# Kernel tuning notes

Hardware: AMD Instinct MI355X
Metric: run time of the kernel (lower is better)

## Reference

```python
import jax, jax.numpy as jnp
import numpy as np
from jax import lax

B, N, T, H, E, D, K = 2, 1024, 4096, 256, 2, 2, 9


def angle2vector(a):
    return jnp.stack([jnp.sin(a), jnp.cos(a)], axis=-1)


def setup_inputs() -> dict:
    key = jax.random.key(0)
    ks = jax.random.split(key, 16)
    s = jnp.float32(0.05)
    return {
        "x": jax.random.normal(ks[0], (B, N, T), jnp.float32),
        "z": jax.random.uniform(ks[1], (B, T, E, D), jnp.float32, 0.0, 2.0 * np.pi),
        # encoder: depthwise conv (groups=N) then two 1x1 convs
        "dw_w": jax.random.normal(ks[2], (N, 1, K), jnp.float32) * s,
        "dw_b": jax.random.normal(ks[3], (N,), jnp.float32) * s,
        "w1": jax.random.normal(ks[4], (H, N), jnp.float32) * s,
        "b1": jax.random.normal(ks[5], (H,), jnp.float32) * s,
        "w2": jax.random.normal(ks[6], (H, H), jnp.float32) * s,
        "b2": jax.random.normal(ks[7], (H,), jnp.float32) * s,
        # heads (1x1 convs)
        "wm": jax.random.normal(ks[8], (E * D * 2, H), jnp.float32) * s,
        "bm": jax.random.normal(ks[9], (E * D * 2,), jnp.float32) * s,
        "wv": jax.random.normal(ks[10], (E * D, H), jnp.float32) * s,
        "bv": jax.random.normal(ks[11], (E * D,), jnp.float32) * s,
        # feature basis / readout params
        "receptive_fields": jax.random.uniform(ks[12], (N, E, D), jnp.float32, 0.0, 2.0 * np.pi),
        "ensemble_weights": jax.random.normal(ks[13], (N, E), jnp.float32),
        "final_scale": jax.random.normal(ks[14], (N,), jnp.float32) * s,
        "log_tuning_width": jnp.full((1,), np.log(2.0), jnp.float32),
    }


def reference(x, z, dw_w, dw_b, w1, b1, w2, b2, wm, bm, wv, bv,
              receptive_fields, ensemble_weights, final_scale, log_tuning_width):
    # ---- encoder ----
    # depthwise conv1d, kernel_size=K, padding='same', groups=N
    h = lax.conv_general_dilated(
        x, dw_w, window_strides=(1,), padding="SAME",
        feature_group_count=N, dimension_numbers=("NCH", "OIH", "NCH"))
    h = h + dw_b[None, :, None]
    h = jax.nn.relu(jnp.einsum("hn,bnt->bht", w1, h) + b1[None, :, None])
    h = jax.nn.relu(jnp.einsum("gh,bht->bgt", w2, h) + b2[None, :, None])

    # ---- heads ----
    mu = jnp.einsum("oh,bht->bot", wm, h) + bm[None, :, None]  # [B, E*D*2, T]
    mu = mu.transpose(0, 2, 1).reshape(B, T, E, D, 2)
    logvar = jnp.einsum("oh,bht->bot", wv, h) + bv[None, :, None]  # [B, E*D, T]
    logvar = logvar.transpose(0, 2, 1).reshape(B, T, E, D)
    # normalize encodings onto unit circle
    mu = mu / jnp.sqrt(jnp.sum(mu ** 2, axis=-1, keepdims=True))

    # ---- feature basis ('bump') ----
    zv = angle2vector(z)                     # [B, T, E, D, 2]
    rfv = angle2vector(receptive_fields)     # [N, E, D, 2]
    diff = zv[:, :, None] - rfv[None, None]  # [B, T, N, E, D, 2]
    dist = jnp.sum(diff ** 2, axis=(4, 5))   # [B, T, N, E]
    response = jnp.exp(-dist / jnp.exp(log_tuning_width))  # nonlinearity='exp'

    # ---- ensemble-weighted readout ----
    ew = jax.nn.softmax(ensemble_weights, axis=1)  # [N, E]
    responses = jnp.einsum("btne,ne->btn", response, ew)
    responses = responses * jnp.exp(final_scale)[None, None]
    responses = responses.transpose(0, 2, 1)  # [B, N, T]
    return responses, z, mu, logvar
```

## Files before the change

kernel.cpp:

```cpp
#include <hip/hip_runtime.h>
#include <hip/hip_bf16.h>

#define B_ 2
#define N_ 1024
#define T_ 4096
#define H_ 256
#define ROWS_ 8192

typedef float f32x4 __attribute__((ext_vector_type(4)));
typedef __bf16 bf16x8 __attribute__((ext_vector_type(8)));

__device__ __forceinline__ void gl16(const void* g, void* l) {
  __builtin_amdgcn_global_load_lds(
      (const __attribute__((address_space(1))) void*)g,
      (__attribute__((address_space(3))) void*)l, 16, 0, 0);
}

__global__ __launch_bounds__(256) void cvt_split(
    const float* __restrict__ w1, const float* __restrict__ w2,
    __bf16* __restrict__ w1h, __bf16* __restrict__ w1l,
    __bf16* __restrict__ w2h, __bf16* __restrict__ w2l) {
  int i = blockIdx.x * 256 + threadIdx.x;
  if (i < 262144) {
    float v = w1[i];
    __bf16 h = (__bf16)v;
    w1h[i] = h;
    w1l[i] = (__bf16)(v - (float)h);
  } else {
    int j = i - 262144;
    float v = w2[j];
    __bf16 h = (__bf16)v;
    w2h[j] = h;
    w2l[j] = (__bf16)(v - (float)h);
  }
}

__global__ __launch_bounds__(256) void dwconv_t(
    const float* __restrict__ x, const float* __restrict__ w,
    const float* __restrict__ bias, __bf16* __restrict__ h0h,
    __bf16* __restrict__ h0l) {
  __shared__ float xs[64][76];
  const int tid = threadIdx.x;
  const int t0 = blockIdx.x * 64;
  const int n0 = blockIdx.y * 64;
  const int b = blockIdx.z;
  for (int i = tid; i < 64 * 72; i += 256) {
    int rr = i / 72, cc = i % 72;
    int tt = t0 - 4 + cc;
    xs[rr][cc] = (tt >= 0 && tt < T_) ? x[((size_t)(b * N_ + n0 + rr)) * T_ + tt] : 0.f;
  }
  const int nl = tid & 63;
  const int tg = tid >> 6;
  float wr[9];
  #pragma unroll
  for (int k = 0; k < 9; ++k) wr[k] = w[(n0 + nl) * 9 + k];
  const float bb = bias[n0 + nl];
  __syncthreads();
  float win[24];
  #pragma unroll
  for (int c = 0; c < 6; ++c)
    *(f32x4*)&win[c * 4] = *(const f32x4*)&xs[nl][tg * 16 + c * 4];
  const size_t obase = ((size_t)b * T_ + t0 + tg * 16) * N_ + n0 + nl;
  #pragma unroll
  for (int j = 0; j < 16; ++j) {
    float acc = bb;
    #pragma unroll
    for (int k = 0; k < 9; ++k) acc = fmaf(win[j + k], wr[k], acc);
    __bf16 h = (__bf16)acc;
    h0h[obase + (size_t)j * N_] = h;
    h0l[obase + (size_t)j * N_] = (__bf16)(acc - (float)h);
  }
}

__global__ __launch_bounds__(512) void encoder_fused(
    const __bf16* __restrict__ Ah, const __bf16* __restrict__ Al,
    const __bf16* __restrict__ W1h, const __bf16* __restrict__ W1l,
    const float* __restrict__ b1,
    const __bf16* __restrict__ W2h, const __bf16* __restrict__ W2l,
    const float* __restrict__ b2,
    const float* __restrict__ wm, const float* __restrict__ bm,
    const float* __restrict__ wv, const float* __restrict__ bv,
    float* __restrict__ out_mu, float* __restrict__ out_lv) {
  __shared__ __attribute__((aligned(16))) char smem[126976];
  char* const ASB = smem;
  char* const WSB = smem + 8192;
  char* const H1B = smem + 73728;
  float* const WMV = (float*)(smem + 106496);
  float* const H2S = (float*)(smem + 8192);

  const int tid = threadIdx.x;
  const int row0 = blockIdx.x * 32;
  const int lane = tid & 63;
  const int wid = tid >> 6;
  const int wt = (wid >> 2) * 16;
  const int wg = (wid & 3) * 64;
  const int lr = lane & 15;
  const int ls = lane >> 4;

  if (tid < 256) {
    #pragma unroll
    for (int i = 0; i < 8; ++i) WMV[tid * 20 + i] = wm[i * 256 + tid];
    #pragma unroll
    for (int i = 0; i < 4; ++i) WMV[tid * 20 + 8 + i] = wv[i * 256 + tid];
  }

  float b1g[4], b2g[4];
  #pragma unroll
  for (int ni = 0; ni < 4; ++ni) {
    b1g[ni] = b1[wg + ni * 16 + lr];
    b2g[ni] = b2[wg + ni * 16 + lr];
  }

  const int a_pl = tid >> 7;
  const int a_idx = tid & 127;
  const int a_r = a_idx >> 2;
  const int a_c = (a_idx & 3) ^ ((a_r >> 1) & 3);
  const __bf16* a_src = (a_pl ? Al : Ah) + (size_t)(row0 + a_r) * 1024 + a_c * 8;
  char* const a_dst = ASB + a_pl * 2048 + a_idx * 16;

  auto STAGE_A = [&](int buf, int kt) {
    if (tid < 256) gl16(a_src + kt * 32, a_dst + buf * 4096);
  };
  auto STAGE_W = [&](int buf, int k0, const __bf16* Wh, const __bf16* Wl, int K) {
    #pragma unroll
    for (int j = 0; j < 4; ++j) {
      const int s = tid + j * 512;
      const int pl = s >> 10;
      const int idx = s & 1023;
      const int g = idx >> 2;
      const int c = (idx & 3) ^ ((g >> 1) & 3);
      gl16((pl ? Wl : Wh) + (size_t)g * K + k0 + c * 8, WSB + buf * 32768 + s * 16);
    }
  };
  auto FR_A = [&](int cur, int pl, int r) {
    return *(const bf16x8*)(ASB + cur * 4096 + pl * 2048 + r * 64 +
                            (ls ^ ((r >> 1) & 3)) * 16);
  };
  auto FR_W = [&](int cur, int pl, int g) {
    return *(const bf16x8*)(WSB + cur * 32768 + pl * 16384 + g * 64 +
                            (ls ^ ((g >> 1) & 3)) * 16);
  };

  f32x4 acc[4];
  #pragma unroll
  for (int i = 0; i < 4; ++i) acc[i] = (f32x4)0.f;

  STAGE_A(0, 0);
  STAGE_W(0, 0, W1h, W1l, 1024);
  __syncthreads();
  for (int kt = 0; kt < 32; ++kt) {
    const int cur = kt & 1;
    if (kt + 1 < 32) {
      STAGE_A(cur ^ 1, kt + 1);
      STAGE_W(cur ^ 1, (kt + 1) * 32, W1h, W1l, 1024);
    }
    bf16x8 ah = FR_A(cur, 0, wt + lr);
    bf16x8 al = FR_A(cur, 1, wt + lr);
    #pragma unroll
    for (int ni = 0; ni < 4; ++ni) {
      bf16x8 wh = FR_W(cur, 0, wg + ni * 16 + lr);
      bf16x8 wl = FR_W(cur, 1, wg + ni * 16 + lr);
      acc[ni] = __builtin_amdgcn_mfma_f32_16x16x32_bf16(ah, wh, acc[ni], 0, 0, 0);
      acc[ni] = __builtin_amdgcn_mfma_f32_16x16x32_bf16(ah, wl, acc[ni], 0, 0, 0);
      acc[ni] = __builtin_amdgcn_mfma_f32_16x16x32_bf16(al, wh, acc[ni], 0, 0, 0);
    }
    __syncthreads();
  }

  #pragma unroll
  for (int ni = 0; ni < 4; ++ni) {
    const int g = wg + ni * 16 + lr;
    const int c = g >> 3;
    #pragma unroll
    for (int reg = 0; reg < 4; ++reg) {
      const int t = wt + ls * 4 + reg;
      float v = fmaxf(acc[ni][reg] + b1g[ni], 0.f);
      __bf16 h = (__bf16)v;
      const int off = t * 512 + ((c ^ (t & 7)) * 16) + (g & 7) * 2;
      *(__bf16*)(H1B + off) = h;
      *(__bf16*)(H1B + 16384 + off) = (__bf16)(v - (float)h);
    }
    acc[ni] = (f32x4)0.f;
  }
  STAGE_W(0, 0, W2h, W2l, 256);
  __syncthreads();

  for (int kt = 0; kt < 8; ++kt) {
    const int cur = kt & 1;
    if (kt + 1 < 8) STAGE_W(cur ^ 1, (kt + 1) * 32, W2h, W2l, 256);
    const int t = wt + lr;
    const int ca = ((kt * 4 + ls) ^ (t & 7)) * 16;
    bf16x8 ah = *(const bf16x8*)(H1B + t * 512 + ca);
    bf16x8 al = *(const bf16x8*)(H1B + 16384 + t * 512 + ca);
    #pragma unroll
    for (int ni = 0; ni < 4; ++ni) {
      bf16x8 wh = FR_W(cur, 0, wg + ni * 16 + lr);
      bf16x8 wl = FR_W(cur, 1, wg + ni * 16 + lr);
      acc[ni] = __builtin_amdgcn_mfma_f32_16x16x32_bf16(ah, wh, acc[ni], 0, 0, 0);
      acc[ni] = __builtin_amdgcn_mfma_f32_16x16x32_bf16(ah, wl, acc[ni], 0, 0, 0);
      acc[ni] = __builtin_amdgcn_mfma_f32_16x16x32_bf16(al, wh, acc[ni], 0, 0, 0);
    }
    __syncthreads();
  }

  #pragma unroll
  for (int ni = 0; ni < 4; ++ni) {
    const int g = wg + ni * 16 + lr;
    #pragma unroll
    for (int reg = 0; reg < 4; ++reg) {
      const int t = wt + ls * 4 + reg;
      H2S[t * 264 + g] = fmaxf(acc[ni][reg] + b2g[ni], 0.f);
    }
  }
  __syncthreads();

  const int ht = tid >> 4;
  const int sub = tid & 15;
  float s[12];
  #pragma unroll
  for (int o = 0; o < 12; ++o) s[o] = 0.f;
  #pragma unroll
  for (int j = 0; j < 16; ++j) {
    const int k = sub + j * 16;
    const float hv = H2S[ht * 264 + k];
    const float* wp = &WMV[k * 20];
    #pragma unroll
    for (int o = 0; o < 12; ++o) s[o] = fmaf(wp[o], hv, s[o]);
  }
  #pragma unroll
  for (int o = 0; o < 12; ++o) {
    s[o] += __shfl_xor(s[o], 1);
    s[o] += __shfl_xor(s[o], 2);
    s[o] += __shfl_xor(s[o], 4);
    s[o] += __shfl_xor(s[o], 8);
  }
  const size_t row = row0 + ht;
  if (sub == 0) {
    float mm[8];
    #pragma unroll
    for (int ed = 0; ed < 4; ++ed) {
      float m0 = s[ed * 2] + bm[ed * 2];
      float m1 = s[ed * 2 + 1] + bm[ed * 2 + 1];
      float inv = 1.f / sqrtf(m0 * m0 + m1 * m1);
      mm[ed * 2] = m0 * inv;
      mm[ed * 2 + 1] = m1 * inv;
    }
    *(float4*)&out_mu[row * 8] = make_float4(mm[0], mm[1], mm[2], mm[3]);
    *(float4*)&out_mu[row * 8 + 4] = make_float4(mm[4], mm[5], mm[6], mm[7]);
  } else if (sub == 1) {
    *(float4*)&out_lv[row * 4] =
        make_float4(s[8] + bv[0], s[9] + bv[1], s[10] + bv[2], s[11] + bv[3]);
  }
}

__global__ __launch_bounds__(256) void resp_kernel(
    const float* __restrict__ z, const float* __restrict__ rf,
    const float* __restrict__ ew, const float* __restrict__ fs,
    const float* __restrict__ ltw, float* __restrict__ out,
    float* __restrict__ out_z) {
  __shared__ float s_sin[32][4], s_cos[32][4], s_w[32][2];
  const int tid = threadIdx.x;
  const int tc = blockIdx.x;
  const int nc = blockIdx.y;
  const int b = blockIdx.z;
  if (tid < 128) {
    int nl = tid >> 2, ed = tid & 3;
    float a = rf[(nc * 32 + nl) * 4 + ed];
    s_sin[nl][ed] = sinf(a);
    s_cos[nl][ed] = cosf(a);
  }
  if (tid < 32) {
    int n = nc * 32 + tid;
    float e0 = ew[n * 2], e1 = ew[n * 2 + 1];
    float m = fmaxf(e0, e1);
    float x0 = expf(e0 - m), x1 = expf(e1 - m);
    float sc = expf(fs[n]) / (x0 + x1);
    s_w[tid][0] = x0 * sc;
    s_w[tid][1] = x1 * sc;
  }
  __syncthreads();
  const int t = tc * 1024 + (tid >> 6) * 256 + (tid & 63) * 4;
  const float inv_tw = expf(-ltw[0]);
  float sz[16], cz[16];
  #pragma unroll
  for (int j = 0; j < 4; ++j) {
    float4 zv = *(const float4*)&z[((size_t)b * T_ + t + j) * 4];
    if (nc == 0) *(float4*)&out_z[((size_t)b * T_ + t + j) * 4] = zv;
    sz[j * 4 + 0] = sinf(zv.x); cz[j * 4 + 0] = cosf(zv.x);
    sz[j * 4 + 1] = sinf(zv.y); cz[j * 4 + 1] = cosf(zv.y);
    sz[j * 4 + 2] = sinf(zv.z); cz[j * 4 + 2] = cosf(zv.z);
    sz[j * 4 + 3] = sinf(zv.w); cz[j * 4 + 3] = cosf(zv.w);
  }
  float* op = out + (size_t)b * N_ * T_ + (size_t)(nc * 32) * T_ + t;
  for (int nl = 0; nl < 32; ++nl) {
    const float ss0 = s_sin[nl][0], sc0 = s_cos[nl][0];
    const float ss1 = s_sin[nl][1], sc1 = s_cos[nl][1];
    const float ss2 = s_sin[nl][2], sc2 = s_cos[nl][2];
    const float ss3 = s_sin[nl][3], sc3 = s_cos[nl][3];
    const float w0 = s_w[nl][0], w1 = s_w[nl][1];
    float o[4];
    #pragma unroll
    for (int j = 0; j < 4; ++j) {
      float d0 = sz[j * 4] * ss0 + cz[j * 4] * sc0 + sz[j * 4 + 1] * ss1 + cz[j * 4 + 1] * sc1;
      float d1 = sz[j * 4 + 2] * ss2 + cz[j * 4 + 2] * sc2 + sz[j * 4 + 3] * ss3 + cz[j * 4 + 3] * sc3;
      float r0 = __expf((2.f * d0 - 4.f) * inv_tw);
      float r1 = __expf((2.f * d1 - 4.f) * inv_tw);
      o[j] = w0 * r0 + w1 * r1;
    }
    *(float4*)&op[(size_t)nl * T_] = make_float4(o[0], o[1], o[2], o[3]);
  }
}

extern "C" void kernel_launch(void* const* d_in, const int* in_sizes, int n_in,
                              void* d_out, int out_size, void* d_ws, size_t ws_size,
                              hipStream_t stream) {
  const float* x   = (const float*)d_in[0];
  const float* z   = (const float*)d_in[1];
  const float* dww = (const float*)d_in[2];
  const float* dwb = (const float*)d_in[3];
  const float* w1  = (const float*)d_in[4];
  const float* b1  = (const float*)d_in[5];
  const float* w2  = (const float*)d_in[6];
  const float* b2  = (const float*)d_in[7];
  const float* wm  = (const float*)d_in[8];
  const float* bm  = (const float*)d_in[9];
  const float* wv  = (const float*)d_in[10];
  const float* bv  = (const float*)d_in[11];
  const float* rf  = (const float*)d_in[12];
  const float* ew  = (const float*)d_in[13];
  const float* fs  = (const float*)d_in[14];
  const float* ltw = (const float*)d_in[15];

  float* out = (float*)d_out;
  float* out_resp = out;
  float* out_z    = out + (size_t)B_ * N_ * T_;
  float* out_mu   = out_z + (size_t)B_ * T_ * 4;
  float* out_lv   = out_mu + (size_t)B_ * T_ * 8;

  __bf16* h0h = (__bf16*)out_resp;
  __bf16* h0l = h0h + (size_t)ROWS_ * N_;

  __bf16* p = (__bf16*)d_ws;
  __bf16* w1h = p; p += 262144;
  __bf16* w1l = p; p += 262144;
  __bf16* w2h = p; p += 65536;
  __bf16* w2l = p; p += 65536;

  cvt_split<<<1280, 256, 0, stream>>>(w1, w2, w1h, w1l, w2h, w2l);
  dwconv_t<<<dim3(T_ / 64, N_ / 64, B_), 256, 0, stream>>>(x, dww, dwb, h0h, h0l);
  encoder_fused<<<dim3(ROWS_ / 32), 512, 0, stream>>>(
      h0h, h0l, w1h, w1l, b1, w2h, w2l, b2, wm, bm, wv, bv, out_mu, out_lv);
  resp_kernel<<<dim3(4, 32, 2), 256, 0, stream>>>(
      z, rf, ew, fs, ltw, out_resp, out_z);
}
```

Baseline: 186.4 us.

## Pre-pack weights into tile order and deepen encoder GEMM prefetch pipeline

The weight split kernel now writes the hi/lo bf16 planes already in the swizzled per-k-tile layout, so each encoder stage loads one contiguous 32KB block with simple offsets instead of computing per-element gather addresses. The encoder GEMM loops move from double-buffered single-step prefetch with __syncthreads to a two-tile-ahead prefetch. They use explicit vmcnt waits and raw s_barrier, so global-to-LDS loads overlap the MFMA work, and s_setprio raises priority around the MFMA block. The hand-counted waitcnt values are fragile and could cause races if the compiler emits a different number of memory ops.

```diff
diff --git a/kernel.cpp b/kernel.cpp
--- a/kernel.cpp
+++ b/kernel.cpp
@@ -16,23 +16,36 @@
       (__attribute__((address_space(3))) void*)l, 16, 0, 0);
 }
 
-__global__ __launch_bounds__(256) void cvt_split(
+#define WAITV(N) asm volatile("s_waitcnt vmcnt(" #N ")" ::: "memory")
+#define FENCE_ALL() asm volatile("s_waitcnt vmcnt(0) lgkmcnt(0)" ::: "memory")
+#define LGKM0() asm volatile("s_waitcnt lgkmcnt(0)" ::: "memory")
+
+__global__ __launch_bounds__(256) void cvt_pack(
     const float* __restrict__ w1, const float* __restrict__ w2,
-    __bf16* __restrict__ w1h, __bf16* __restrict__ w1l,
-    __bf16* __restrict__ w2h, __bf16* __restrict__ w2l) {
-  int i = blockIdx.x * 256 + threadIdx.x;
-  if (i < 262144) {
-    float v = w1[i];
+    __bf16* __restrict__ w1p, __bf16* __restrict__ w2p) {
+  const int i = blockIdx.x * 256 + threadIdx.x;
+  const float* src;
+  __bf16* dst;
+  int K, kt, s;
+  if (i < 65536) {
+    kt = i >> 11; s = i & 2047; src = w1; K = 1024; dst = w1p + (size_t)i * 8;
+  } else {
+    int j = i - 65536;
+    kt = j >> 11; s = j & 2047; src = w2; K = 256; dst = w2p + (size_t)j * 8;
+  }
+  const int pl = s >> 10;
+  const int idx = s & 1023;
+  const int g = idx >> 2;
+  const int cc = (idx & 3) ^ ((g >> 1) & 3);
+  const float* p = src + (size_t)g * K + kt * 32 + cc * 8;
+  bf16x8 o;
+  #pragma unroll
+  for (int e = 0; e < 8; ++e) {
+    float v = p[e];
     __bf16 h = (__bf16)v;
-    w1h[i] = h;
-    w1l[i] = (__bf16)(v - (float)h);
-  } else {
-    int j = i - 262144;
-    float v = w2[j];
-    __bf16 h = (__bf16)v;
-    w2h[j] = h;
-    w2l[j] = (__bf16)(v - (float)h);
-  }
+    o[e] = pl ? (__bf16)(v - (float)h) : h;
+  }
+  *(bf16x8*)dst = o;
 }
 
 __global__ __launch_bounds__(256) void dwconv_t(
@@ -74,10 +87,8 @@
 
 __global__ __launch_bounds__(512) void encoder_fused(
     const __bf16* __restrict__ Ah, const __bf16* __restrict__ Al,
-    const __bf16* __restrict__ W1h, const __bf16* __restrict__ W1l,
-    const float* __restrict__ b1,
-    const __bf16* __restrict__ W2h, const __bf16* __restrict__ W2l,
-    const float* __restrict__ b2,
+    const __bf16* __restrict__ W1P, const float* __restrict__ b1,
+    const __bf16* __restrict__ W2P, const float* __restrict__ b2,
     const float* __restrict__ wm, const float* __restrict__ bm,
     const float* __restrict__ wv, const float* __restrict__ bv,
     float* __restrict__ out_mu, float* __restrict__ out_lv) {
@@ -103,13 +114,13 @@
     #pragma unroll
     for (int i = 0; i < 4; ++i) WMV[tid * 20 + 8 + i] = wv[i * 256 + tid];
   }
-
   float b1g[4], b2g[4];
   #pragma unroll
   for (int ni = 0; ni < 4; ++ni) {
     b1g[ni] = b1[wg + ni * 16 + lr];
     b2g[ni] = b2[wg + ni * 16 + lr];
   }
+  FENCE_ALL();
 
   const int a_pl = tid >> 7;
   const int a_idx = tid & 127;
@@ -121,16 +132,11 @@
   auto STAGE_A = [&](int buf, int kt) {
     if (tid < 256) gl16(a_src + kt * 32, a_dst + buf * 4096);
   };
-  auto STAGE_W = [&](int buf, int k0, const __bf16* Wh, const __bf16* Wl, int K) {
-    #pragma unroll
-    for (int j = 0; j < 4; ++j) {
-      const int s = tid + j * 512;
-      const int pl = s >> 10;
-      const int idx = s & 1023;
-      const int g = idx >> 2;
-      const int c = (idx & 3) ^ ((g >> 1) & 3);
-      gl16((pl ? Wl : Wh) + (size_t)g * K + k0 + c * 8, WSB + buf * 32768 + s * 16);
-    }
+  auto STAGE_W = [&](int buf, int kt, const __bf16* WP) {
+    const char* src = (const char*)WP + (size_t)kt * 32768 + tid * 16;
+    char* dst = WSB + buf * 32768 + tid * 16;
+    #pragma unroll
+    for (int j = 0; j < 4; ++j) gl16(src + j * 8192, dst + j * 8192);
   };
   auto FR_A = [&](int cur, int pl, int r) {
     return *(const bf16x8*)(ASB + cur * 4096 + pl * 2048 + r * 64 +
@@ -145,26 +151,35 @@
   #pragma unroll
   for (int i = 0; i < 4; ++i) acc[i] = (f32x4)0.f;
 
-  STAGE_A(0, 0);
-  STAGE_W(0, 0, W1h, W1l, 1024);
-  __syncthreads();
+  STAGE_A(0, 0); STAGE_W(0, 0, W1P);
+  STAGE_A(1, 1); STAGE_W(1, 1, W1P);
   for (int kt = 0; kt < 32; ++kt) {
     const int cur = kt & 1;
-    if (kt + 1 < 32) {
-      STAGE_A(cur ^ 1, kt + 1);
-      STAGE_W(cur ^ 1, (kt + 1) * 32, W1h, W1l, 1024);
-    }
-    bf16x8 ah = FR_A(cur, 0, wt + lr);
-    bf16x8 al = FR_A(cur, 1, wt + lr);
-    #pragma unroll
-    for (int ni = 0; ni < 4; ++ni) {
-      bf16x8 wh = FR_W(cur, 0, wg + ni * 16 + lr);
-      bf16x8 wl = FR_W(cur, 1, wg + ni * 16 + lr);
-      acc[ni] = __builtin_amdgcn_mfma_f32_16x16x32_bf16(ah, wh, acc[ni], 0, 0, 0);
-      acc[ni] = __builtin_amdgcn_mfma_f32_16x16x32_bf16(ah, wl, acc[ni], 0, 0, 0);
-      acc[ni] = __builtin_amdgcn_mfma_f32_16x16x32_bf16(al, wh, acc[ni], 0, 0, 0);
-    }
-    __syncthreads();
+    if (kt < 31) {
+      if (tid < 256) WAITV(5); else WAITV(4);
+    } else {
+      WAITV(0);
+    }
+    __builtin_amdgcn_s_barrier();
+    {
+      const int ra = wt + lr;
+      bf16x8 ah = FR_A(cur, 0, ra);
+      bf16x8 al = FR_A(cur, 1, ra);
+      __builtin_amdgcn_s_setprio(1);
+      #pragma unroll
+      for (int ni = 0; ni < 4; ++ni) {
+        const int rw = wg + ni * 16 + lr;
+        bf16x8 wh = FR_W(cur, 0, rw);
+        bf16x8 wl = FR_W(cur, 1, rw);
+        acc[ni] = __builtin_amdgcn_mfma_f32_16x16x32_bf16(ah, wh, acc[ni], 0, 0, 0);
+        acc[ni] = __builtin_amdgcn_mfma_f32_16x16x32_bf16(ah, wl, acc[ni], 0, 0, 0);
+        acc[ni] = __builtin_amdgcn_mfma_f32_16x16x32_bf16(al, wh, acc[ni], 0, 0, 0);
+      }
+      __builtin_amdgcn_s_setprio(0);
+    }
+    LGKM0();
+    __builtin_amdgcn_s_barrier();
+    if (kt < 30) { STAGE_A(cur, kt + 2); STAGE_W(cur, kt + 2, W1P); }
   }
 
   #pragma unroll
@@ -182,25 +197,34 @@
     }
     acc[ni] = (f32x4)0.f;
   }
-  STAGE_W(0, 0, W2h, W2l, 256);
-  __syncthreads();
-
+
+  STAGE_W(0, 0, W2P);
+  STAGE_W(1, 1, W2P);
   for (int kt = 0; kt < 8; ++kt) {
     const int cur = kt & 1;
-    if (kt + 1 < 8) STAGE_W(cur ^ 1, (kt + 1) * 32, W2h, W2l, 256);
-    const int t = wt + lr;
-    const int ca = ((kt * 4 + ls) ^ (t & 7)) * 16;
-    bf16x8 ah = *(const bf16x8*)(H1B + t * 512 + ca);
-    bf16x8 al = *(const bf16x8*)(H1B + 16384 + t * 512 + ca);
-    #pragma unroll
-    for (int ni = 0; ni < 4; ++ni) {
-      bf16x8 wh = FR_W(cur, 0, wg + ni * 16 + lr);
-      bf16x8 wl = FR_W(cur, 1, wg + ni * 16 + lr);
-      acc[ni] = __builtin_amdgcn_mfma_f32_16x16x32_bf16(ah, wh, acc[ni], 0, 0, 0);
-      acc[ni] = __builtin_amdgcn_mfma_f32_16x16x32_bf16(ah, wl, acc[ni], 0, 0, 0);
-      acc[ni] = __builtin_amdgcn_mfma_f32_16x16x32_bf16(al, wh, acc[ni], 0, 0, 0);
-    }
-    __syncthreads();
+    if (kt < 7) WAITV(4); else WAITV(0);
+    LGKM0();
+    __builtin_amdgcn_s_barrier();
+    {
+      const int t = wt + lr;
+      const int ca = ((kt * 4 + ls) ^ (t & 7)) * 16;
+      bf16x8 ah = *(const bf16x8*)(H1B + t * 512 + ca);
+      bf16x8 al = *(const bf16x8*)(H1B + 16384 + t * 512 + ca);
+      __builtin_amdgcn_s_setprio(1);
+      #pragma unroll
+      for (int ni = 0; ni < 4; ++ni) {
+        const int rw = wg + ni * 16 + lr;
+        bf16x8 wh = FR_W(cur, 0, rw);
+        bf16x8 wl = FR_W(cur, 1, rw);
+        acc[ni] = __builtin_amdgcn_mfma_f32_16x16x32_bf16(ah, wh, acc[ni], 0, 0, 0);
+        acc[ni] = __builtin_amdgcn_mfma_f32_16x16x32_bf16(ah, wl, acc[ni], 0, 0, 0);
+        acc[ni] = __builtin_amdgcn_mfma_f32_16x16x32_bf16(al, wh, acc[ni], 0, 0, 0);
+      }
+      __builtin_amdgcn_s_setprio(0);
+    }
+    LGKM0();
+    __builtin_amdgcn_s_barrier();
+    if (kt < 6) STAGE_W(cur, kt + 2, W2P);
   }
 
   #pragma unroll
@@ -212,7 +236,8 @@
       H2S[t * 264 + g] = fmaxf(acc[ni][reg] + b2g[ni], 0.f);
     }
   }
-  __syncthreads();
+  LGKM0();
+  __builtin_amdgcn_s_barrier();
 
   const int ht = tid >> 4;
   const int sub = tid & 15;
@@ -341,15 +366,13 @@
   __bf16* h0l = h0h + (size_t)ROWS_ * N_;
 
   __bf16* p = (__bf16*)d_ws;
-  __bf16* w1h = p; p += 262144;
-  __bf16* w1l = p; p += 262144;
-  __bf16* w2h = p; p += 65536;
-  __bf16* w2l = p; p += 65536;
-
-  cvt_split<<<1280, 256, 0, stream>>>(w1, w2, w1h, w1l, w2h, w2l);
+  __bf16* w1p = p; p += 524288;
+  __bf16* w2p = p; p += 131072;
+
+  cvt_pack<<<320, 256, 0, stream>>>(w1, w2, w1p, w2p);
   dwconv_t<<<dim3(T_ / 64, N_ / 64, B_), 256, 0, stream>>>(x, dww, dwb, h0h, h0l);
   encoder_fused<<<dim3(ROWS_ / 32), 512, 0, stream>>>(
-      h0h, h0l, w1h, w1l, b1, w2h, w2l, b2, wm, bm, wv, bv, out_mu, out_lv);
+      h0h, h0l, w1p, b1, w2p, b2, wm, bm, wv, bv, out_mu, out_lv);
   resp_kernel<<<dim3(4, 32, 2), 256, 0, stream>>>(
       z, rf, ew, fs, ltw, out_resp, out_z);
 }
```

After: 175.8 us. 5.7% less time.
